# Performance work log

Hardware: AMD Instinct MI355X
Metric: run time of the kernel (lower is better)

The kernel has to match this reference:

```python
import jax, jax.numpy as jnp
import numpy as np
import math

B, L, E, H = 512, 200, 64, 4
D = E // H
NEG = jnp.float32(-(2.0 ** 32) + 1.0)


def setup_inputs() -> dict:
    key = jax.random.key(0)
    ks = jax.random.split(key, 12)
    inp = jax.random.normal(ks[0], (B, L, E), dtype=jnp.float32)
    # realistic variable-length histories: mask[b, t] = t < len_b, len_b in [1, L]
    lens = jax.random.randint(ks[1], (B, 1), 1, L + 1)
    mask = jnp.arange(L)[None, :] < lens  # [B, L] bool
    s = 1.0 / math.sqrt(E)
    pos_enc = jax.random.normal(ks[2], (1, L, E), dtype=jnp.float32)
    Wk = jax.random.uniform(ks[3], (E, E), jnp.float32, -s, s)
    bk = jnp.zeros((E,), jnp.float32)
    Wv = jax.random.uniform(ks[4], (E, E), jnp.float32, -s, s)
    bv = jnp.zeros((E,), jnp.float32)
    Wq = jax.random.uniform(ks[5], (E, E), jnp.float32, -s, s)
    bq = jnp.zeros((E,), jnp.float32)
    Wf = jax.random.uniform(ks[6], (E, E), jnp.float32, -s, s)
    bf = jnp.zeros((E,), jnp.float32)
    return {"input": inp, "mask": mask, "pos_enc": pos_enc,
            "Wk": Wk, "bk": bk, "Wv": Wv, "bv": bv,
            "Wq": Wq, "bq": bq, "Wf": Wf, "bf": bf}


def reference(input, mask, pos_enc, Wk, bk, Wv, bv, Wq, bq, Wf, bf):
    x = input + pos_enc  # [B, L, E]
    # project and split heads: [B, H, L, D]
    def split(t):
        return t.reshape(B, L, H, D).transpose(0, 2, 1, 3)
    k = split(x @ Wk.T + bk)
    v = split(x @ Wv.T + bv)
    q = split(x @ Wq.T + bq) / math.sqrt(D)
    scores = jnp.einsum('bhqd,bhkd->bhqk', q, k)  # [B, H, L, L]
    # key_mask in torch code broadcasts over dim 3 (mask on the QUERY axis),
    # query_mask is its transpose (mask on the KEY axis). Combined: both must be valid.
    both = mask[:, None, :, None] & mask[:, None, None, :]  # [B, 1, L, L]
    scores = jnp.where(both, scores, NEG)
    attn = jax.nn.softmax(scores, axis=-1)
    # dropout is identity at inference; omitted deterministically
    out = jnp.einsum('bhqk,bhkd->bhqd', attn, v)
    out = out.transpose(0, 2, 1, 3).reshape(B, L, E)
    out = out @ Wf.T + bf
    fm = mask.astype(jnp.float32)[:, :, None]  # [B, L, 1]
    lens = jnp.sum(fm, axis=1)  # [B, 1]
    pooled = jnp.sum(out * fm, axis=1) / (lens + 1e-8)  # [B, E]
    return pooled
```

## Files before the change

### kernel.cpp

```cpp
#include <hip/hip_runtime.h>
#include <hip/hip_fp16.h>
#include <math.h>

#define Bn 512
#define Ln 200
#define En 64
#define Hn 4
#define Dn 16
#define KS3 18
#define VS3 200
#define QSC 0.36067376022224085f

typedef _Float16 __f16;
typedef __fp16 fp16x2 __attribute__((ext_vector_type(2)));
typedef __f16 f16x4 __attribute__((ext_vector_type(4)));
typedef __f16 f16x8 __attribute__((ext_vector_type(8)));
typedef float f32x4 __attribute__((ext_vector_type(4)));

#if __has_builtin(__builtin_amdgcn_exp2f)
__device__ __forceinline__ float fexp2(float x) { return __builtin_amdgcn_exp2f(x); }
#else
__device__ __forceinline__ float fexp2(float x) { return exp2f(x); }
#endif

__device__ __forceinline__ f16x8 pack8s(float4 a, float4 b, float4 pa, float4 pb) {
    f16x8 r;
    r[0] = (__f16)(a.x + pa.x); r[1] = (__f16)(a.y + pa.y);
    r[2] = (__f16)(a.z + pa.z); r[3] = (__f16)(a.w + pa.w);
    r[4] = (__f16)(b.x + pb.x); r[5] = (__f16)(b.y + pb.y);
    r[6] = (__f16)(b.z + pb.z); r[7] = (__f16)(b.w + pb.w);
    return r;
}
__device__ __forceinline__ f16x8 pack8(float4 a, float4 b) {
    f16x8 r;
    r[0] = (__f16)a.x; r[1] = (__f16)a.y; r[2] = (__f16)a.z; r[3] = (__f16)a.w;
    r[4] = (__f16)b.x; r[5] = (__f16)b.y; r[6] = (__f16)b.z; r[7] = (__f16)b.w;
    return r;
}

__device__ __forceinline__ f16x4 pack4rtz(float e0, float e1, float e2, float e3) {
    const fp16x2 lo = __builtin_amdgcn_cvt_pkrtz(e0, e1);
    const fp16x2 hi = __builtin_amdgcn_cvt_pkrtz(e2, e3);
    f16x4 r;
    r[0] = (__f16)lo[0]; r[1] = (__f16)lo[1];
    r[2] = (__f16)hi[0]; r[3] = (__f16)hi[1];
    return r;
}

template<int NI>
__device__ __forceinline__ void attn_core(
    const __f16* __restrict__ Kh_, const __f16* __restrict__ Qh_, const __f16* __restrict__ Vt_,
    int qt0, int klo, int khi, int nt, int len, int quad, int ln16,
    f32x4 (&o2)[4], f32x4 (&lacc)[4])
{
    const f16x4 ones = {(__f16)1.f, (__f16)1.f, (__f16)1.f, (__f16)1.f};
    f16x4 qf[NI];
    #pragma unroll
    for (int i = 0; i < NI; ++i) {
        int qr = min((qt0 + i) * 16 + ln16, Ln - 1);
        qf[i] = *(const f16x4*)(Qh_ + qr * KS3 + quad * 4);
    }
    const bool needmask = (khi == nt);
    const int kfull = khi - (needmask ? 1 : 0);

    f16x4 kf = *(const f16x4*)(Kh_ + min(klo * 16 + ln16, Ln - 1) * KS3 + quad * 4);
    f16x4 vf = *(const f16x4*)(Vt_ + ln16 * VS3 + min(klo * 16 + quad * 4, Ln - 4));

    for (int kt = klo; kt < kfull; ++kt) {
        const int krn = min((kt + 1) * 16 + ln16, Ln - 1);
        const int vcn = min((kt + 1) * 16 + quad * 4, Ln - 4);
        const f16x4 kfn = *(const f16x4*)(Kh_ + krn * KS3 + quad * 4);
        const f16x4 vfn = *(const f16x4*)(Vt_ + ln16 * VS3 + vcn);
        f32x4 s[NI];
        #pragma unroll
        for (int i = 0; i < NI; ++i)
            s[i] = __builtin_amdgcn_mfma_f32_16x16x16f16(kf, qf[i], (f32x4){0,0,0,0}, 0, 0, 0);
        f16x4 pf[NI];
        #pragma unroll
        for (int i = 0; i < NI; ++i) {
            pf[i] = pack4rtz(fexp2(fminf(s[i][0], 14.5f)),
                             fexp2(fminf(s[i][1], 14.5f)),
                             fexp2(fminf(s[i][2], 14.5f)),
                             fexp2(fminf(s[i][3], 14.5f)));
        }
        #pragma unroll
        for (int i = 0; i < NI; ++i) {
            o2[i]   = __builtin_amdgcn_mfma_f32_16x16x16f16(vf,   pf[i], o2[i],   0, 0, 0);
            lacc[i] = __builtin_amdgcn_mfma_f32_16x16x16f16(ones, pf[i], lacc[i], 0, 0, 0);
        }
        kf = kfn; vf = vfn;
    }
    if (needmask) {
        const int kbase = (nt - 1) * 16 + quad * 4;
        f32x4 s[NI];
        #pragma unroll
        for (int i = 0; i < NI; ++i)
            s[i] = __builtin_amdgcn_mfma_f32_16x16x16f16(kf, qf[i], (f32x4){0,0,0,0}, 0, 0, 0);
        f16x4 pf[NI];
        #pragma unroll
        for (int i = 0; i < NI; ++i) {
            float e[4];
            #pragma unroll
            for (int j = 0; j < 4; ++j) {
                const bool kok = (kbase + j) < len;
                e[j] = kok ? fexp2(fminf(s[i][j], 14.5f)) : 0.f;
            }
            pf[i] = pack4rtz(e[0], e[1], e[2], e[3]);
        }
        #pragma unroll
        for (int i = 0; i < NI; ++i) {
            o2[i]   = __builtin_amdgcn_mfma_f32_16x16x16f16(vf,   pf[i], o2[i],   0, 0, 0);
            lacc[i] = __builtin_amdgcn_mfma_f32_16x16x16f16(ones, pf[i], lacc[i], 0, 0, 0);
        }
    }
}

__global__ __launch_bounds__(256, 4) void fused_kernel(
    const float* __restrict__ input, const int* __restrict__ mask,
    const float* __restrict__ pos_enc,
    const float* __restrict__ Wk, const float* __restrict__ bk,
    const float* __restrict__ Wv, const float* __restrict__ bv,
    const float* __restrict__ Wq, const float* __restrict__ bq,
    const float* __restrict__ Wf, const float* __restrict__ bf_,
    float* __restrict__ out)
{
    __shared__ __align__(16) __f16 Kh[Ln * KS3];
    __shared__ __align__(16) __f16 Qh[Ln * KS3];
    __shared__ __align__(16) __f16 Vt[16 * VS3];
    __shared__ float lred[4][4][16];
    __shared__ float red[4][16];
    __shared__ float ph[16];
    __shared__ int cnt_red[4];

    const int tid  = threadIdx.x;
    const int lin  = ((blockIdx.x & 7) << 8) | (blockIdx.x >> 3);
    const int b    = lin >> 2, h = lin & 3;
    const int wave = tid >> 6, lane = tid & 63;
    const int quad = lane >> 4, ln16 = lane & 15;

    const float4* in4 = (const float4*)(input + (size_t)b * Ln * En);
    const float4* pe4 = (const float4*)pos_enc;

    float4 px0, px1, px2, px3;
    {
        const int o4 = (wave * 16 + ln16) * 16 + quad * 2;
        px0 = in4[o4];     px1 = in4[o4 + 1];
        px2 = in4[o4 + 8]; px3 = in4[o4 + 9];
    }

    const int mv = (tid < Ln) ? mask[b * Ln + tid] : 0;

    f16x8 bfr[3][2];
    #pragma unroll
    for (int m = 0; m < 3; ++m) {
        const float* W = (m == 0) ? Wk : (m == 1) ? Wv : Wq;
        #pragma unroll
        for (int ks = 0; ks < 2; ++ks) {
            const float4* wp = (const float4*)(W + (size_t)(h * 16 + ln16) * 64) + (ks * 8 + quad * 2);
            bfr[m][ks] = pack8(wp[0], wp[1]);
        }
    }
    const int cg = h * 16 + ln16;
    const float bkv = bk[cg], bvv = bv[cg], bqv = bq[cg];

    int c = (mv != 0) ? 1 : 0;
    #pragma unroll
    for (int off = 32; off; off >>= 1) c += __shfl_down(c, off, 64);
    if (lane == 0) cnt_red[wave] = c;
    __syncthreads();
    const int len = cnt_red[0] + cnt_red[1] + cnt_red[2] + cnt_red[3];
    const int nt = (len + 15) >> 4;

    for (int rt = wave; rt < nt; rt += 4) {
        const int R = rt * 16 + ln16;
        const bool rok = (R < Ln);
        const int o4 = R * 16 + quad * 2;

        const int rtn = rt + 4;
        const int Rn = rtn * 16 + ln16;
        float4 pxn0 = {0,0,0,0}, pxn1 = {0,0,0,0}, pxn2 = {0,0,0,0}, pxn3 = {0,0,0,0};
        if (rtn < nt && Rn < Ln) {
            const int o4n = Rn * 16 + quad * 2;
            pxn0 = in4[o4n];     pxn1 = in4[o4n + 1];
            pxn2 = in4[o4n + 8]; pxn3 = in4[o4n + 9];
        }
        float4 pp0 = {0,0,0,0}, pp1 = {0,0,0,0}, pp2 = {0,0,0,0}, pp3 = {0,0,0,0};
        if (rok) {
            pp0 = pe4[o4];     pp1 = pe4[o4 + 1];
            pp2 = pe4[o4 + 8]; pp3 = pe4[o4 + 9];
        }
        f16x8 af0 = pack8s(px0, px1, pp0, pp1);
        f16x8 af1 = pack8s(px2, px3, pp2, pp3);

        f32x4 acc[3];
        #pragma unroll
        for (int m = 0; m < 3; ++m) acc[m] = (f32x4){0,0,0,0};
        #pragma unroll
        for (int m = 0; m < 3; ++m)
            acc[m] = __builtin_amdgcn_mfma_f32_16x16x32_f16(af0, bfr[m][0], acc[m], 0, 0, 0);
        #pragma unroll
        for (int m = 0; m < 3; ++m)
            acc[m] = __builtin_amdgcn_mfma_f32_16x16x32_f16(af1, bfr[m][1], acc[m], 0, 0, 0);

        #pragma unroll
        for (int j = 0; j < 4; ++j) {
            const int t = rt * 16 + quad * 4 + j;
            if (t < Ln) {
                Kh[t * KS3 + ln16] = (__f16)(acc[0][j] + bkv);
                Qh[t * KS3 + ln16] = (__f16)((acc[2][j] + bqv) * QSC);
            }
        }
        const int vc0 = rt * 16 + quad * 4;
        if (vc0 < Ln) {
            f16x4 vp;
            #pragma unroll
            for (int j = 0; j < 4; ++j) vp[j] = (__f16)(acc[1][j] + bvv);
            *(f16x4*)(Vt + ln16 * VS3 + vc0) = vp;
        }
        px0 = pxn0; px1 = pxn1; px2 = pxn2; px3 = pxn3;
    }
    __syncthreads();

    const int nquad = (nt + 3) >> 2;
    int g, kh, nkh;
    if (nquad >= 3)      { g = wave;     kh = 0;         nkh = 1; }
    else if (nquad == 2) { g = wave & 1; kh = wave >> 1; nkh = 2; }
    else                 { g = 0;        kh = wave;      nkh = 4; }
    const bool active = (g < nquad);
    const int nktp = (nt + nkh - 1) / nkh;
    const int klo = kh * nktp;
    const int khi = min(klo + nktp, nt);
    const int qt0 = 4 * g;

    f32x4 o2[4], lacc[4];
    #pragma unroll
    for (int i = 0; i < 4; ++i) { o2[i] = (f32x4){0,0,0,0}; lacc[i] = (f32x4){0,0,0,0}; }

    if (active && klo < khi) {
        const int ni = __builtin_amdgcn_readfirstlane(min(4, nt - qt0));
        switch (ni) {
            case 1:  attn_core<1>(Kh, Qh, Vt, qt0, klo, khi, nt, len, quad, ln16, o2, lacc); break;
            case 2:  attn_core<2>(Kh, Qh, Vt, qt0, klo, khi, nt, len, quad, ln16, o2, lacc); break;
            case 3:  attn_core<3>(Kh, Qh, Vt, qt0, klo, khi, nt, len, quad, ln16, o2, lacc); break;
            default: attn_core<4>(Kh, Qh, Vt, qt0, klo, khi, nt, len, quad, ln16, o2, lacc); break;
        }
    }

    float l[4];
    #pragma unroll
    for (int i = 0; i < 4; ++i) l[i] = lacc[i][0];

    if (nkh > 1) {
        if (lane < 16) {
            #pragma unroll
            for (int i = 0; i < 4; ++i) lred[wave][i][lane] = l[i];
        }
        __syncthreads();
        #pragma unroll
        for (int i = 0; i < 4; ++i) {
            if (nkh == 2) l[i] = lred[g][i][ln16] + lred[g + 2][i][ln16];
            else          l[i] = lred[0][i][ln16] + lred[1][i][ln16]
                               + lred[2][i][ln16] + lred[3][i][ln16];
        }
    }

    f32x4 pool = {0.f, 0.f, 0.f, 0.f};
    if (active) {
        #pragma unroll
        for (int i = 0; i < 4; ++i) {
            const float rs = ((qt0 + i) * 16 + ln16 < len) ? 1.f / l[i] : 0.f;
            #pragma unroll
            for (int j = 0; j < 4; ++j) pool[j] = fmaf(o2[i][j], rs, pool[j]);
        }
    }

    #pragma unroll
    for (int j = 0; j < 4; ++j) {
        #pragma unroll
        for (int off = 1; off < 16; off <<= 1) pool[j] += __shfl_xor(pool[j], off, 64);
    }
    if (ln16 == 0) {
        #pragma unroll
        for (int j = 0; j < 4; ++j) red[wave][quad * 4 + j] = pool[j];
    }
    __syncthreads();
    if (tid < 16)
        ph[tid] = (red[0][tid] + red[1][tid] + red[2][tid] + red[3][tid]) / ((float)len + 1e-8f);
    __syncthreads();

    if (tid < 64) {
        const int e = tid;
        const float* wr = Wf + (size_t)e * 64 + h * 16;
        float a = (h == 0) ? bf_[e] : 0.f;
        #pragma unroll
        for (int i = 0; i < 16; ++i) a = fmaf(wr[i], ph[i], a);
        atomicAdd(out + b * En + e, a);
    }
}

extern "C" void kernel_launch(void* const* d_in, const int* in_sizes, int n_in,
                              void* d_out, int out_size, void* d_ws, size_t ws_size,
                              hipStream_t stream) {
    const float* input   = (const float*)d_in[0];
    const int*   mask    = (const int*)  d_in[1];
    const float* pos_enc = (const float*)d_in[2];
    const float* Wk      = (const float*)d_in[3];
    const float* bk      = (const float*)d_in[4];
    const float* Wv      = (const float*)d_in[5];
    const float* bv      = (const float*)d_in[6];
    const float* Wq      = (const float*)d_in[7];
    const float* bq      = (const float*)d_in[8];
    const float* Wf      = (const float*)d_in[9];
    const float* bf      = (const float*)d_in[10];

    float* out = (float*)d_out;
    hipMemsetAsync(out, 0, (size_t)Bn * En * sizeof(float), stream);

    fused_kernel<<<Bn * Hn, 256, 0, stream>>>(input, mask, pos_enc,
                                              Wk, bk, Wv, bv, Wq, bq, Wf, bf, out);
}
```

Before: 122.0 us.

## Split fused attention into per-batch projection and per-head attention kernels

Adds a projection kernel that computes K, Q and V for all four heads of a batch element in one block and writes fp16 tiles to a global workspace. A separate attention kernel then reads them per (batch, head) without LDS staging. The goal is to stop re-reading the input once per head (four times overall) and to shrink the fused kernel's LDS footprint. In exchange it adds a global round trip and a second launch, and the attention kernel now reads K/Q/V from global memory instead of LDS. The old fused path stays as a fallback when the workspace is too small, and its first input load is now gated by the sequence length.

Measured after the change: 136.6 us. 12.0% more time.

```diff
diff --git a/kernel.cpp b/kernel.cpp
--- a/kernel.cpp
+++ b/kernel.cpp
@@ -6,9 +6,11 @@
 #define Ln 200
 #define En 64
 #define Hn 4
-#define Dn 16
+#define ITEMS (Bn * Hn)
+#define TSZ 3200
 #define KS3 18
-#define VS3 200
+#define KSG 16
+#define VS 200
 #define QSC 0.36067376022224085f
 
 typedef _Float16 __f16;
@@ -37,7 +39,6 @@
     r[4] = (__f16)b.x; r[5] = (__f16)b.y; r[6] = (__f16)b.z; r[7] = (__f16)b.w;
     return r;
 }
-
 __device__ __forceinline__ f16x4 pack4rtz(float e0, float e1, float e2, float e3) {
     const fp16x2 lo = __builtin_amdgcn_cvt_pkrtz(e0, e1);
     const fp16x2 hi = __builtin_amdgcn_cvt_pkrtz(e2, e3);
@@ -47,7 +48,7 @@
     return r;
 }
 
-template<int NI>
+template<int NI, int KS_>
 __device__ __forceinline__ void attn_core(
     const __f16* __restrict__ Kh_, const __f16* __restrict__ Qh_, const __f16* __restrict__ Vt_,
     int qt0, int klo, int khi, int nt, int len, int quad, int ln16,
@@ -58,19 +59,19 @@
     #pragma unroll
     for (int i = 0; i < NI; ++i) {
         int qr = min((qt0 + i) * 16 + ln16, Ln - 1);
-        qf[i] = *(const f16x4*)(Qh_ + qr * KS3 + quad * 4);
+        qf[i] = *(const f16x4*)(Qh_ + qr * KS_ + quad * 4);
     }
     const bool needmask = (khi == nt);
     const int kfull = khi - (needmask ? 1 : 0);
 
-    f16x4 kf = *(const f16x4*)(Kh_ + min(klo * 16 + ln16, Ln - 1) * KS3 + quad * 4);
-    f16x4 vf = *(const f16x4*)(Vt_ + ln16 * VS3 + min(klo * 16 + quad * 4, Ln - 4));
+    f16x4 kf = *(const f16x4*)(Kh_ + min(klo * 16 + ln16, Ln - 1) * KS_ + quad * 4);
+    f16x4 vf = *(const f16x4*)(Vt_ + ln16 * VS + min(klo * 16 + quad * 4, Ln - 4));
 
     for (int kt = klo; kt < kfull; ++kt) {
         const int krn = min((kt + 1) * 16 + ln16, Ln - 1);
         const int vcn = min((kt + 1) * 16 + quad * 4, Ln - 4);
-        const f16x4 kfn = *(const f16x4*)(Kh_ + krn * KS3 + quad * 4);
-        const f16x4 vfn = *(const f16x4*)(Vt_ + ln16 * VS3 + vcn);
+        const f16x4 kfn = *(const f16x4*)(Kh_ + krn * KS_ + quad * 4);
+        const f16x4 vfn = *(const f16x4*)(Vt_ + ln16 * VS + vcn);
         f32x4 s[NI];
         #pragma unroll
         for (int i = 0; i < NI; ++i)
@@ -112,6 +113,229 @@
             o2[i]   = __builtin_amdgcn_mfma_f32_16x16x16f16(vf,   pf[i], o2[i],   0, 0, 0);
             lacc[i] = __builtin_amdgcn_mfma_f32_16x16x16f16(ones, pf[i], lacc[i], 0, 0, 0);
         }
+    }
+}
+
+__global__ __launch_bounds__(256, 2) void proj_kernel(
+    const float* __restrict__ input, const int* __restrict__ mask,
+    const float* __restrict__ pos_enc,
+    const float* __restrict__ Wk, const float* __restrict__ bk,
+    const float* __restrict__ Wv, const float* __restrict__ bv,
+    const float* __restrict__ Wq, const float* __restrict__ bq,
+    __f16* __restrict__ ws)
+{
+    const int tid  = threadIdx.x;
+    const int b    = blockIdx.x;
+    const int wv   = tid >> 6, lane = tid & 63;
+    const int quad = lane >> 4, ln16 = lane & 15;
+
+    const float4* in4 = (const float4*)(input + (size_t)b * Ln * En);
+    const float4* pe4 = (const float4*)pos_enc;
+
+    const int* mb = mask + b * Ln;
+    int c = (mb[lane] != 0) + (mb[64 + lane] != 0) + (mb[128 + lane] != 0)
+          + ((lane < Ln - 192) ? (mb[192 + lane] != 0) : 0);
+    #pragma unroll
+    for (int off = 32; off; off >>= 1) c += __shfl_down(c, off, 64);
+    const int len = __shfl(c, 0, 64);
+    const int nt = (len + 15) >> 4;
+
+    f16x8 bfr[3][4][2];
+    float bz[3][4];
+    #pragma unroll
+    for (int m = 0; m < 3; ++m) {
+        const float* W = (m == 0) ? Wk : (m == 1) ? Wv : Wq;
+        const float* B = (m == 0) ? bk : (m == 1) ? bv : bq;
+        #pragma unroll
+        for (int h = 0; h < 4; ++h) {
+            #pragma unroll
+            for (int ks = 0; ks < 2; ++ks) {
+                const float4* wp = (const float4*)(W + (size_t)(h * 16 + ln16) * 64) + (ks * 8 + quad * 2);
+                bfr[m][h][ks] = pack8(wp[0], wp[1]);
+            }
+            bz[m][h] = B[h * 16 + ln16];
+        }
+    }
+
+    __f16* Kg = ws;
+    __f16* Qg = ws + (size_t)ITEMS * TSZ;
+    __f16* Vg = ws + (size_t)2 * ITEMS * TSZ;
+
+#define LDX(rt, A0, A1, A2, A3)                                        \
+    {                                                                  \
+        A0 = A1 = A2 = A3 = (float4){0, 0, 0, 0};                      \
+        const int R_ = (rt) * 16 + ln16;                               \
+        if ((rt) < nt && R_ < Ln) {                                    \
+            const int o4_ = R_ * 16 + quad * 2;                        \
+            A0 = in4[o4_];     A1 = in4[o4_ + 1];                      \
+            A2 = in4[o4_ + 8]; A3 = in4[o4_ + 9];                      \
+        }                                                              \
+    }
+
+    float4 c0, c1, c2, c3, n0, n1, n2, n3, t0, t1, t2, t3;
+    LDX(wv,     c0, c1, c2, c3);
+    LDX(wv + 4, n0, n1, n2, n3);
+
+    for (int rt = wv; rt < nt; rt += 4) {
+        LDX(rt + 8, t0, t1, t2, t3);
+
+        const int R = rt * 16 + ln16;
+        const bool rok = (R < Ln);
+        const int o4 = R * 16 + quad * 2;
+        float4 p0 = {0,0,0,0}, p1 = {0,0,0,0}, p2 = {0,0,0,0}, p3 = {0,0,0,0};
+        if (rok) {
+            p0 = pe4[o4];     p1 = pe4[o4 + 1];
+            p2 = pe4[o4 + 8]; p3 = pe4[o4 + 9];
+        }
+        const f16x8 af0 = pack8s(c0, c1, p0, p1);
+        const f16x8 af1 = pack8s(c2, c3, p2, p3);
+
+        f32x4 acc[3][4];
+        #pragma unroll
+        for (int m = 0; m < 3; ++m)
+            #pragma unroll
+            for (int h = 0; h < 4; ++h)
+                acc[m][h] = (f32x4){bz[m][h], bz[m][h], bz[m][h], bz[m][h]};
+        #pragma unroll
+        for (int m = 0; m < 3; ++m)
+            #pragma unroll
+            for (int h = 0; h < 4; ++h)
+                acc[m][h] = __builtin_amdgcn_mfma_f32_16x16x32_f16(af0, bfr[m][h][0], acc[m][h], 0, 0, 0);
+        #pragma unroll
+        for (int m = 0; m < 3; ++m)
+            #pragma unroll
+            for (int h = 0; h < 4; ++h)
+                acc[m][h] = __builtin_amdgcn_mfma_f32_16x16x32_f16(af1, bfr[m][h][1], acc[m][h], 0, 0, 0);
+
+        #pragma unroll
+        for (int j = 0; j < 4; ++j) {
+            const int t = rt * 16 + quad * 4 + j;
+            if (t < Ln) {
+                #pragma unroll
+                for (int h = 0; h < 4; ++h) {
+                    const size_t base = (size_t)(b * 4 + h) * TSZ + t * KSG + ln16;
+                    Kg[base] = (__f16)acc[0][h][j];
+                    Qg[base] = (__f16)(acc[2][h][j] * QSC);
+                }
+            }
+        }
+        const int vc0 = rt * 16 + quad * 4;
+        if (vc0 < Ln) {
+            #pragma unroll
+            for (int h = 0; h < 4; ++h) {
+                f16x4 vp;
+                #pragma unroll
+                for (int j = 0; j < 4; ++j) vp[j] = (__f16)acc[1][h][j];
+                *(f16x4*)(Vg + (size_t)(b * 4 + h) * TSZ + ln16 * VS + vc0) = vp;
+            }
+        }
+        c0 = n0; c1 = n1; c2 = n2; c3 = n3;
+        n0 = t0; n1 = t1; n2 = t2; n3 = t3;
+    }
+#undef LDX
+}
+
+__global__ __launch_bounds__(256, 4) void attn_kernel(
+    const int* __restrict__ mask, const __f16* __restrict__ ws,
+    const float* __restrict__ Wf, const float* __restrict__ bf_,
+    float* __restrict__ out)
+{
+    __shared__ float lred[4][4][16];
+    __shared__ float red[4][16];
+    __shared__ float ph[16];
+
+    const int tid  = threadIdx.x;
+    const int item = blockIdx.x;
+    const int b    = item >> 2, h = item & 3;
+    const int wave = tid >> 6, lane = tid & 63;
+    const int quad = lane >> 4, ln16 = lane & 15;
+
+    const int* mb = mask + b * Ln;
+    int c = (mb[lane] != 0) + (mb[64 + lane] != 0) + (mb[128 + lane] != 0)
+          + ((lane < Ln - 192) ? (mb[192 + lane] != 0) : 0);
+    #pragma unroll
+    for (int off = 32; off; off >>= 1) c += __shfl_down(c, off, 64);
+    const int len = __shfl(c, 0, 64);
+    const int nt = (len + 15) >> 4;
+
+    const __f16* Kg = ws + (size_t)item * TSZ;
+    const __f16* Qg = ws + (size_t)ITEMS * TSZ + (size_t)item * TSZ;
+    const __f16* Vg = ws + (size_t)2 * ITEMS * TSZ + (size_t)item * TSZ;
+
+    const int nquad = (nt + 3) >> 2;
+    int g, kh, nkh;
+    if (nquad >= 3)      { g = wave;     kh = 0;         nkh = 1; }
+    else if (nquad == 2) { g = wave & 1; kh = wave >> 1; nkh = 2; }
+    else                 { g = 0;        kh = wave;      nkh = 4; }
+    const bool active = (g < nquad);
+    const int nktp = (nt + nkh - 1) / nkh;
+    const int klo = kh * nktp;
+    const int khi = min(klo + nktp, nt);
+    const int qt0 = 4 * g;
+
+    f32x4 o2[4], lacc[4];
+    #pragma unroll
+    for (int i = 0; i < 4; ++i) { o2[i] = (f32x4){0,0,0,0}; lacc[i] = (f32x4){0,0,0,0}; }
+
+    if (active && klo < khi) {
+        const int ni = __builtin_amdgcn_readfirstlane(min(4, nt - qt0));
+        switch (ni) {
+            case 1:  attn_core<1, KSG>(Kg, Qg, Vg, qt0, klo, khi, nt, len, quad, ln16, o2, lacc); break;
+            case 2:  attn_core<2, KSG>(Kg, Qg, Vg, qt0, klo, khi, nt, len, quad, ln16, o2, lacc); break;
+            case 3:  attn_core<3, KSG>(Kg, Qg, Vg, qt0, klo, khi, nt, len, quad, ln16, o2, lacc); break;
+            default: attn_core<4, KSG>(Kg, Qg, Vg, qt0, klo, khi, nt, len, quad, ln16, o2, lacc); break;
+        }
+    }
+
+    float l[4];
+    #pragma unroll
+    for (int i = 0; i < 4; ++i) l[i] = lacc[i][0];
+
+    if (nkh > 1) {
+        if (lane < 16) {
+            #pragma unroll
+            for (int i = 0; i < 4; ++i) lred[wave][i][lane] = l[i];
+        }
+        __syncthreads();
+        #pragma unroll
+        for (int i = 0; i < 4; ++i) {
+            if (nkh == 2) l[i] = lred[g][i][ln16] + lred[g + 2][i][ln16];
+            else          l[i] = lred[0][i][ln16] + lred[1][i][ln16]
+                               + lred[2][i][ln16] + lred[3][i][ln16];
+        }
+    }
+
+    f32x4 pool = {0.f, 0.f, 0.f, 0.f};
+    if (active) {
+        #pragma unroll
+        for (int i = 0; i < 4; ++i) {
+            const float rs = ((qt0 + i) * 16 + ln16 < len) ? 1.f / l[i] : 0.f;
+            #pragma unroll
+            for (int j = 0; j < 4; ++j) pool[j] = fmaf(o2[i][j], rs, pool[j]);
+        }
+    }
+
+    #pragma unroll
+    for (int j = 0; j < 4; ++j) {
+        #pragma unroll
+        for (int off = 1; off < 16; off <<= 1) pool[j] += __shfl_xor(pool[j], off, 64);
+    }
+    if (ln16 == 0) {
+        #pragma unroll
+        for (int j = 0; j < 4; ++j) red[wave][quad * 4 + j] = pool[j];
+    }
+    __syncthreads();
+    if (tid < 16)
+        ph[tid] = (red[0][tid] + red[1][tid] + red[2][tid] + red[3][tid]) / ((float)len + 1e-8f);
+    __syncthreads();
+
+    if (tid < 64) {
+        const int e = tid;
+        const float* wr = Wf + (size_t)e * 64 + h * 16;
+        float a = (h == 0) ? bf_[e] : 0.f;
+        #pragma unroll
+        for (int i = 0; i < 16; ++i) a = fmaf(wr[i], ph[i], a);
+        atomicAdd(out + b * En + e, a);
     }
 }
 
@@ -126,7 +350,7 @@
 {
     __shared__ __align__(16) __f16 Kh[Ln * KS3];
     __shared__ __align__(16) __f16 Qh[Ln * KS3];
-    __shared__ __align__(16) __f16 Vt[16 * VS3];
+    __shared__ __align__(16) __f16 Vt[16 * VS];
     __shared__ float lred[4][4][16];
     __shared__ float red[4][16];
     __shared__ float ph[16];
@@ -141,13 +365,12 @@
     const float4* in4 = (const float4*)(input + (size_t)b * Ln * En);
     const float4* pe4 = (const float4*)pos_enc;
 
-    float4 px0, px1, px2, px3;
-    {
-        const int o4 = (wave * 16 + ln16) * 16 + quad * 2;
+    float4 px0 = {0,0,0,0}, px1 = {0,0,0,0}, px2 = {0,0,0,0}, px3 = {0,0,0,0};
+    if (wave == 0) {
+        const int o4 = ln16 * 16 + quad * 2;
         px0 = in4[o4];     px1 = in4[o4 + 1];
         px2 = in4[o4 + 8]; px3 = in4[o4 + 9];
     }
-
     const int mv = (tid < Ln) ? mask[b * Ln + tid] : 0;
 
     f16x8 bfr[3][2];
@@ -171,11 +394,16 @@
     const int len = cnt_red[0] + cnt_red[1] + cnt_red[2] + cnt_red[3];
     const int nt = (len + 15) >> 4;
 
+    if (wave != 0 && wave < nt) {
+        const int o4 = (wave * 16 + ln16) * 16 + quad * 2;
+        px0 = in4[o4];     px1 = in4[o4 + 1];
+        px2 = in4[o4 + 8]; px3 = in4[o4 + 9];
+    }
+
     for (int rt = wave; rt < nt; rt += 4) {
         const int R = rt * 16 + ln16;
         const bool rok = (R < Ln);
         const int o4 = R * 16 + quad * 2;
-
         const int rtn = rt + 4;
         const int Rn = rtn * 16 + ln16;
         float4 pxn0 = {0,0,0,0}, pxn1 = {0,0,0,0}, pxn2 = {0,0,0,0}, pxn3 = {0,0,0,0};
@@ -189,8 +417,8 @@
             pp0 = pe4[o4];     pp1 = pe4[o4 + 1];
             pp2 = pe4[o4 + 8]; pp3 = pe4[o4 + 9];
         }
-        f16x8 af0 = pack8s(px0, px1, pp0, pp1);
-        f16x8 af1 = pack8s(px2, px3, pp2, pp3);
+        const f16x8 af0 = pack8s(px0, px1, pp0, pp1);
+        const f16x8 af1 = pack8s(px2, px3, pp2, pp3);
 
         f32x4 acc[3];
         #pragma unroll
@@ -215,7 +443,7 @@
             f16x4 vp;
             #pragma unroll
             for (int j = 0; j < 4; ++j) vp[j] = (__f16)(acc[1][j] + bvv);
-            *(f16x4*)(Vt + ln16 * VS3 + vc0) = vp;
+            *(f16x4*)(Vt + ln16 * VS + vc0) = vp;
         }
         px0 = pxn0; px1 = pxn1; px2 = pxn2; px3 = pxn3;
     }
@@ -239,10 +467,10 @@
     if (active && klo < khi) {
         const int ni = __builtin_amdgcn_readfirstlane(min(4, nt - qt0));
         switch (ni) {
-            case 1:  attn_core<1>(Kh, Qh, Vt, qt0, klo, khi, nt, len, quad, ln16, o2, lacc); break;
-            case 2:  attn_core<2>(Kh, Qh, Vt, qt0, klo, khi, nt, len, quad, ln16, o2, lacc); break;
-            case 3:  attn_core<3>(Kh, Qh, Vt, qt0, klo, khi, nt, len, quad, ln16, o2, lacc); break;
-            default: attn_core<4>(Kh, Qh, Vt, qt0, klo, khi, nt, len, quad, ln16, o2, lacc); break;
+            case 1:  attn_core<1, KS3>(Kh, Qh, Vt, qt0, klo, khi, nt, len, quad, ln16, o2, lacc); break;
+            case 2:  attn_core<2, KS3>(Kh, Qh, Vt, qt0, klo, khi, nt, len, quad, ln16, o2, lacc); break;
+            case 3:  attn_core<3, KS3>(Kh, Qh, Vt, qt0, klo, khi, nt, len, quad, ln16, o2, lacc); break;
+            default: attn_core<4, KS3>(Kh, Qh, Vt, qt0, klo, khi, nt, len, quad, ln16, o2, lacc); break;
         }
     }
 
@@ -316,6 +544,14 @@
     float* out = (float*)d_out;
     hipMemsetAsync(out, 0, (size_t)Bn * En * sizeof(float), stream);
 
-    fused_kernel<<<Bn * Hn, 256, 0, stream>>>(input, mask, pos_enc,
-                                              Wk, bk, Wv, bv, Wq, bq, Wf, bf, out);
-}
+    const size_t need = (size_t)3 * ITEMS * TSZ * sizeof(__f16);
+    if (ws_size >= need) {
+        __f16* ws = (__f16*)d_ws;
+        proj_kernel<<<Bn, 256, 0, stream>>>(input, mask, pos_enc,
+                                            Wk, bk, Wv, bv, Wq, bq, ws);
+        attn_kernel<<<ITEMS, 256, 0, stream>>>(mask, ws, Wf, bf, out);
+    } else {
+        fused_kernel<<<ITEMS, 256, 0, stream>>>(input, mask, pos_enc,
+                                                Wk, bk, Wv, bv, Wq, bq, Wf, bf, out);
+    }
+}
```
